# Performance work log

Hardware: AMD Instinct MI355X
Metric: run time of the kernel (lower is better)

The kernel has to match this reference:

```python
import jax, jax.numpy as jnp
import numpy as np

K = 20          # neighbors per point (knn includes the point itself, as in PyG knn)
EPS = 1e-5      # BatchNorm eps (eval mode, running stats)


def _lrelu(x):
    return jax.nn.leaky_relu(x, 0.2)


def _bn(x, g, beta, mu, var):
    # eval-mode BatchNorm1d over last (feature) axis
    return (x - mu) * (g * jax.lax.rsqrt(var + EPS)) + beta


def _edge_conv(x, W, g, beta, mu, var):
    # x: [B, N, F]. Dynamic kNN graph per batch element, edge feature [x_i, x_j - x_i],
    # Linear(no bias) -> BN -> LeakyReLU(0.2), max-aggregate over neighbors.
    sq = jnp.sum(x * x, axis=-1)                                   # [B, N]
    d2 = sq[:, :, None] + sq[:, None, :] - 2.0 * jnp.einsum('bnf,bmf->bnm', x, x)
    _, idx = jax.lax.top_k(-d2, K)                                 # [B, N, K] (self is nearest)
    xj = jax.vmap(lambda xb, ib: xb[ib])(x, idx)                   # [B, N, K, F]
    xi = jnp.broadcast_to(x[:, :, None, :], xj.shape)
    e = jnp.concatenate([xi, xj - xi], axis=-1) @ W                # [B, N, K, out]
    return jnp.max(_lrelu(_bn(e, g, beta, mu, var)), axis=2)       # [B, N, out]


def setup_inputs() -> dict:
    key = jax.random.key(0)
    ks = iter(jax.random.split(key, 64))
    B, N = 8, 2048
    d = {"pos": jax.random.normal(next(ks), (B, N, 3), jnp.float32)}

    def bn_params(name, dim):
        d["g" + name] = 0.5 + jax.random.uniform(next(ks), (dim,), jnp.float32)
        d["beta" + name] = 0.1 * jax.random.normal(next(ks), (dim,), jnp.float32)
        d["mu" + name] = 0.1 * jax.random.normal(next(ks), (dim,), jnp.float32)
        d["var" + name] = 0.5 + jax.random.uniform(next(ks), (dim,), jnp.float32)

    def lin(name, din, dout):
        d["W" + name] = jax.random.normal(next(ks), (din, dout), jnp.float32) / np.sqrt(din).astype(np.float32)

    lin("1", 2 * 3, 64);    bn_params("1", 64)
    lin("2", 2 * 64, 64);   bn_params("2", 64)
    lin("3", 2 * 64, 128);  bn_params("3", 128)
    lin("4", 2 * 128, 256); bn_params("4", 256)
    lin("m", 512, 1024);    bn_params("m", 1024)
    lin("a", 2048, 512);    bn_params("a", 512)
    lin("b", 512, 256);     bn_params("b", 256)
    d["bias_b"] = 0.01 * jax.random.normal(next(ks), (256,), jnp.float32)
    lin("c", 256, 40)
    d["bias_c"] = 0.01 * jax.random.normal(next(ks), (40,), jnp.float32)
    return d


def reference(pos, W1, g1, beta1, mu1, var1, W2, g2, beta2, mu2, var2,
              W3, g3, beta3, mu3, var3, W4, g4, beta4, mu4, var4,
              Wm, gm, betam, mum, varm, Wa, ga, betaa, mua, vara,
              Wb, gb, betab, mub, varb, bias_b, Wc, bias_c):
    x1 = _edge_conv(pos, W1, g1, beta1, mu1, var1)   # [B, N, 64]
    x2 = _edge_conv(x1, W2, g2, beta2, mu2, var2)    # [B, N, 64]
    x3 = _edge_conv(x2, W3, g3, beta3, mu3, var3)    # [B, N, 128]
    x4 = _edge_conv(x3, W4, g4, beta4, mu4, var4)    # [B, N, 256]
    h = jnp.concatenate([x1, x2, x3, x4], axis=-1)   # [B, N, 512]
    h = _lrelu(_bn(h @ Wm, gm, betam, mum, varm))    # [B, N, 1024]
    pooled = jnp.concatenate([jnp.max(h, axis=1), jnp.mean(h, axis=1)], axis=-1)  # [B, 2048]
    h = _lrelu(_bn(pooled @ Wa, ga, betaa, mua, vara))            # [B, 512]
    h = _lrelu(_bn(h @ Wb + bias_b, gb, betab, mub, varb))        # [B, 256]
    return h @ Wc + bias_c                                        # [B, 40]
```

## Files before the change

### kernel.cpp

```cpp
#include <hip/hip_runtime.h>
#include <cstdint>
#include <cstddef>

#define NPTS 2048
#define BATCH 8
#define KNN 20
#define BIGF 3.402823466e38f

typedef short bf16x8 __attribute__((ext_vector_type(8)));
typedef float f32x4 __attribute__((ext_vector_type(4)));

__device__ __forceinline__ unsigned short f2bf(float v) {
    uint32_t u = __float_as_uint(v);
    uint32_t r = (u + 0x7FFFu + ((u >> 16) & 1u)) >> 16;
    return (unsigned short)r;
}
__device__ __forceinline__ float bf2f(unsigned short h) {
    return __uint_as_float(((uint32_t)h) << 16);
}
__device__ __forceinline__ uint32_t flipkey(float d) {
    uint32_t u = __float_as_uint(d);
    return (u & 0x80000000u) ? ~u : (u | 0x80000000u);
}
__device__ __forceinline__ uint64_t shfl_xor_u64(uint64_t v, int m) {
    int lo = __shfl_xor((int)(uint32_t)v, m, 64);
    int hi = __shfl_xor((int)(uint32_t)(v >> 32), m, 64);
    return ((uint64_t)(uint32_t)hi << 32) | (uint32_t)lo;
}

__global__ __launch_bounds__(256) void sq_kernel(const float* __restrict__ x, int lda, int F,
                                                 float* __restrict__ sq)
{
    int p = blockIdx.x * 256 + threadIdx.x;
    const float* xp = x + (size_t)p * lda;
    float s = 0.f;
    for (int f = 0; f < F; ++f) { float v = xp[f]; s = fmaf(v, v, s); }
    sq[p] = s;
}

__global__ __launch_bounds__(256) void distk_kernel(const float* __restrict__ x, int lda,
                                                    const float* __restrict__ sq,
                                                    uint32_t* __restrict__ d2k, int F, int b0)
{
    __shared__ __align__(16) float As[8][132];
    __shared__ __align__(16) float Bs[8][132];
    const int b  = b0 + blockIdx.z;
    const int i0 = blockIdx.x * 128;
    const int j0 = blockIdx.y * 128;
    const float* xb  = x + (size_t)b * NPTS * lda;
    const float* sqb = sq + (size_t)b * NPTS;
    const int t  = threadIdx.x;
    const int tx = t & 15, ty = t >> 4;
    const int lrow = t >> 1, lkq = (t & 1) * 4;

    float acc[8][8];
#pragma unroll
    for (int r = 0; r < 8; ++r)
#pragma unroll
        for (int c = 0; c < 8; ++c) acc[r][c] = 0.f;

    for (int k0 = 0; k0 < F; k0 += 8) {
        const float* sa = xb + (size_t)(i0 + lrow) * lda + k0 + lkq;
        const float* sb = xb + (size_t)(j0 + lrow) * lda + k0 + lkq;
        if (k0 + 8 <= F) {
            float4 a4 = *reinterpret_cast<const float4*>(sa);
            float4 b4 = *reinterpret_cast<const float4*>(sb);
            As[lkq + 0][lrow] = a4.x; As[lkq + 1][lrow] = a4.y;
            As[lkq + 2][lrow] = a4.z; As[lkq + 3][lrow] = a4.w;
            Bs[lkq + 0][lrow] = b4.x; Bs[lkq + 1][lrow] = b4.y;
            Bs[lkq + 2][lrow] = b4.z; Bs[lkq + 3][lrow] = b4.w;
        } else {
#pragma unroll
            for (int q = 0; q < 4; ++q) {
                int kk = k0 + lkq + q;
                As[lkq + q][lrow] = (kk < F) ? sa[q] : 0.f;
                Bs[lkq + q][lrow] = (kk < F) ? sb[q] : 0.f;
            }
        }
        __syncthreads();
#pragma unroll
        for (int k = 0; k < 8; ++k) {
            float4 a0 = *reinterpret_cast<const float4*>(&As[k][ty * 4]);
            float4 a1 = *reinterpret_cast<const float4*>(&As[k][64 + ty * 4]);
            float4 c0 = *reinterpret_cast<const float4*>(&Bs[k][tx * 4]);
            float4 c1 = *reinterpret_cast<const float4*>(&Bs[k][64 + tx * 4]);
            float av[8] = {a0.x, a0.y, a0.z, a0.w, a1.x, a1.y, a1.z, a1.w};
            float bv[8] = {c0.x, c0.y, c0.z, c0.w, c1.x, c1.y, c1.z, c1.w};
#pragma unroll
            for (int r = 0; r < 8; ++r)
#pragma unroll
                for (int c = 0; c < 8; ++c) acc[r][c] = fmaf(av[r], bv[c], acc[r][c]);
        }
        __syncthreads();
    }

    uint32_t* db = d2k + (size_t)blockIdx.z * NPTS * NPTS;
#pragma unroll
    for (int r = 0; r < 8; ++r) {
        int i = i0 + ((r < 4) ? (ty * 4 + r) : (64 + ty * 4 + r - 4));
        float si = sqb[i];
#pragma unroll
        for (int cq = 0; cq < 2; ++cq) {
            int j = j0 + (cq ? 64 : 0) + tx * 4;
            uint4 o;
            o.x = flipkey(si + sqb[j + 0] - 2.f * acc[r][cq * 4 + 0]);
            o.y = flipkey(si + sqb[j + 1] - 2.f * acc[r][cq * 4 + 1]);
            o.z = flipkey(si + sqb[j + 2] - 2.f * acc[r][cq * 4 + 2]);
            o.w = flipkey(si + sqb[j + 3] - 2.f * acc[r][cq * 4 + 3]);
            *reinterpret_cast<uint4*>(&db[(size_t)i * NPTS + j]) = o;
        }
    }
}

__global__ __launch_bounds__(256) void select_kernel(const uint32_t* __restrict__ d2k,
                                                     int* __restrict__ idx, int b0)
{
    const int t    = threadIdx.x;
    const int lane = t & 63;
    const int wid  = t >> 6;
    const int row_id = blockIdx.x * 4 + wid;
    const int bz = row_id >> 11;
    const int i  = row_id & 2047;
    const uint32_t* row = d2k + ((size_t)bz * NPTS + i) * NPTS;

    uint32_t key[32];
#pragma unroll
    for (int s = 0; s < 8; ++s) {
        uint4 kv = *reinterpret_cast<const uint4*>(&row[s * 256 + lane * 4]);
        key[s * 4 + 0] = kv.x; key[s * 4 + 1] = kv.y;
        key[s * 4 + 2] = kv.z; key[s * 4 + 3] = kv.w;
    }

    const uint64_t MAXV = ~0ull;
    uint64_t t1 = MAXV, t2 = MAXV, t3 = MAXV, t4 = MAXV;

#pragma unroll
    for (int s = 0; s < 8; ++s)
#pragma unroll
        for (int q = 0; q < 4; ++q) {
            uint64_t c = ((uint64_t)key[s * 4 + q] << 32) | (uint32_t)(s * 256 + lane * 4 + q);
            if (c < t4) {
                if (c < t2) {
                    t4 = t3; t3 = t2;
                    if (c < t1) { t2 = t1; t1 = c; } else t2 = c;
                } else {
                    if (c < t3) { t4 = t3; t3 = c; } else t4 = c;
                }
            }
        }

    uint64_t keep = 0;
    for (int it = 0; it < KNN; ++it) {
        uint64_t w = t1;
#pragma unroll
        for (int o = 1; o < 64; o <<= 1) {
            uint64_t ov = shfl_xor_u64(w, o);
            w = (ov < w) ? ov : w;
        }
        keep = (lane == it) ? w : keep;
        if (t1 == w) {
            t1 = t2; t2 = t3; t3 = t4; t4 = MAXV;
            if (t1 == MAXV) {
#pragma unroll
                for (int s = 0; s < 8; ++s)
#pragma unroll
                    for (int q = 0; q < 4; ++q) {
                        uint64_t c = ((uint64_t)key[s * 4 + q] << 32) |
                                     (uint32_t)(s * 256 + lane * 4 + q);
                        if (c > w && c < t4) {
                            if (c < t2) {
                                t4 = t3; t3 = t2;
                                if (c < t1) { t2 = t1; t1 = c; } else t2 = c;
                            } else {
                                if (c < t3) { t4 = t3; t3 = c; } else t4 = c;
                            }
                        }
                    }
            }
        }
    }

    int* out = idx + ((size_t)(b0 + bz) * NPTS + i) * KNN;
    if (lane < KNN) out[lane] = (int)(uint32_t)keep;
}

__global__ __launch_bounds__(256) void gemm64_kernel(const float* __restrict__ A, int lda, int F,
                                                     const float* __restrict__ Wfull, int Fout,
                                                     float* __restrict__ apart,
                                                     float* __restrict__ bpart)
{
    __shared__ float As[16][65];
    __shared__ float Bs[16][65];
    const int i0 = blockIdx.x * 64, j0 = blockIdx.y * 64;
    const int half = blockIdx.z;
    const float* Bw = Wfull + (size_t)(half ? F : 0) * Fout;
    float* C = half ? bpart : apart;
    const int t = threadIdx.x, tx = t & 15, ty = t >> 4;
    float acc[4][4];
#pragma unroll
    for (int r = 0; r < 4; ++r)
#pragma unroll
        for (int c = 0; c < 4; ++c) acc[r][c] = 0.f;
    const int arow = t >> 2, akq = (t & 3) * 4;
    const int bk = t >> 4, bj = (t & 15) * 4;
    for (int k0 = 0; k0 < F; k0 += 16) {
#pragma unroll
        for (int q = 0; q < 4; ++q) {
            int kk = k0 + akq + q;
            As[akq + q][arow] = (kk < F) ? A[(size_t)(i0 + arow) * lda + kk] : 0.f;
        }
        {
            int kk = k0 + bk;
#pragma unroll
            for (int q = 0; q < 4; ++q)
                Bs[bk][bj + q] = (kk < F) ? Bw[(size_t)kk * Fout + j0 + bj + q] : 0.f;
        }
        __syncthreads();
#pragma unroll
        for (int k = 0; k < 16; ++k) {
            float a[4], bb[4];
#pragma unroll
            for (int r = 0; r < 4; ++r) a[r] = As[k][ty * 4 + r];
#pragma unroll
            for (int c = 0; c < 4; ++c) bb[c] = Bs[k][tx * 4 + c];
#pragma unroll
            for (int r = 0; r < 4; ++r)
#pragma unroll
                for (int c = 0; c < 4; ++c) acc[r][c] = fmaf(a[r], bb[c], acc[r][c]);
        }
        __syncthreads();
    }
#pragma unroll
    for (int r = 0; r < 4; ++r)
#pragma unroll
        for (int c = 0; c < 4; ++c)
            C[(size_t)(i0 + ty * 4 + r) * Fout + j0 + tx * 4 + c] = acc[r][c];
}

template <int FOUT>
__global__ __launch_bounds__(256) void aggregate_kernel(const float* __restrict__ apart,
                                                        const float* __restrict__ bpart,
                                                        const int* __restrict__ idx,
                                                        const float* __restrict__ g,
                                                        const float* __restrict__ be,
                                                        const float* __restrict__ mu,
                                                        const float* __restrict__ var,
                                                        float* __restrict__ out)
{
    constexpr int G   = FOUT / 4;
    constexpr int PPB = 256 / G;
    const int t  = threadIdx.x;
    const int pi = t / G;
    const int fi = t % G;
    const int p  = blockIdx.x * PPB + pi;
    const int b  = p >> 11;
    const int* nb = idx + (size_t)p * KNN;
    const float4* bp4 = reinterpret_cast<const float4*>(bpart);
    const float4* bb  = bp4 + ((size_t)b << 11) * G;

    float4 m = {-BIGF, -BIGF, -BIGF, -BIGF};
#pragma unroll 4
    for (int k = 0; k < KNN; ++k) {
        int j = nb[k];
        float4 v = bb[(size_t)j * G + fi];
        m.x = fmaxf(m.x, v.x); m.y = fmaxf(m.y, v.y);
        m.z = fmaxf(m.z, v.z); m.w = fmaxf(m.w, v.w);
    }
    float4 av = reinterpret_cast<const float4*>(apart)[(size_t)p * G + fi];
    float4 bv = bp4[(size_t)p * G + fi];
    float4 gg = reinterpret_cast<const float4*>(g)[fi];
    float4 bee = reinterpret_cast<const float4*>(be)[fi];
    float4 muu = reinterpret_cast<const float4*>(mu)[fi];
    float4 vaa = reinterpret_cast<const float4*>(var)[fi];

    float4 r;
    {
        float s, sh, vv, y;
        s = gg.x * rsqrtf(vaa.x + 1e-5f); sh = bee.x - muu.x * s;
        vv = av.x - bv.x + m.x; y = vv * s + sh; r.x = (y >= 0.f) ? y : 0.2f * y;
        s = gg.y * rsqrtf(vaa.y + 1e-5f); sh = bee.y - muu.y * s;
        vv = av.y - bv.y + m.y; y = vv * s + sh; r.y = (y >= 0.f) ? y : 0.2f * y;
        s = gg.z * rsqrtf(vaa.z + 1e-5f); sh = bee.z - muu.z * s;
        vv = av.z - bv.z + m.z; y = vv * s + sh; r.z = (y >= 0.f) ? y : 0.2f * y;
        s = gg.w * rsqrtf(vaa.w + 1e-5f); sh = bee.w - muu.w * s;
        vv = av.w - bv.w + m.w; y = vv * s + sh; r.w = (y >= 0.f) ? y : 0.2f * y;
    }
    *reinterpret_cast<float4*>(out + (size_t)p * 512 + fi * 4) = r;
}

__global__ __launch_bounds__(256) void cvt_kernel(const float* __restrict__ in,
                                                  unsigned short* __restrict__ hi,
                                                  unsigned short* __restrict__ lo)
{
    int i = blockIdx.x * 256 + threadIdx.x;
    const float4* p = reinterpret_cast<const float4*>(in) + (size_t)i * 2;
    float4 a = p[0], b = p[1];
    float v[8] = {a.x, a.y, a.z, a.w, b.x, b.y, b.z, b.w};
    uint32_t h[8], l[8];
#pragma unroll
    for (int q = 0; q < 8; ++q) {
        unsigned short hb = f2bf(v[q]);
        h[q] = hb;
        l[q] = f2bf(v[q] - bf2f(hb));
    }
    uint4 uh, ul;
    uh.x = h[0] | (h[1] << 16); uh.y = h[2] | (h[3] << 16);
    uh.z = h[4] | (h[5] << 16); uh.w = h[6] | (h[7] << 16);
    ul.x = l[0] | (l[1] << 16); ul.y = l[2] | (l[3] << 16);
    ul.z = l[4] | (l[5] << 16); ul.w = l[6] | (l[7] << 16);
    reinterpret_cast<uint4*>(hi)[i] = uh;
    reinterpret_cast<uint4*>(lo)[i] = ul;
}

__global__ __launch_bounds__(256) void cvtT_kernel(const float* __restrict__ Wm,
                                                   unsigned short* __restrict__ hiT,
                                                   unsigned short* __restrict__ loT)
{
    __shared__ float tile[32][33];
    const int n0 = blockIdx.x * 32;
    const int k0 = blockIdx.y * 32;
    const int t = threadIdx.x;
    const int c = t & 31, r = t >> 5;
#pragma unroll
    for (int rr = 0; rr < 4; ++rr)
        tile[r + rr * 8][c] = Wm[(size_t)(k0 + r + rr * 8) * 1024 + n0 + c];
    __syncthreads();
#pragma unroll
    for (int rr = 0; rr < 4; ++rr) {
        int nn = r + rr * 8, kk = c;
        float v = tile[kk][nn];
        unsigned short hb = f2bf(v);
        hiT[(size_t)(n0 + nn) * 512 + k0 + kk] = hb;
        loT[(size_t)(n0 + nn) * 512 + k0 + kk] = f2bf(v - bf2f(hb));
    }
}

__global__ __launch_bounds__(256) void wm_mfma_pool(const unsigned short* __restrict__ AH,
                                                    const unsigned short* __restrict__ AL,
                                                    const unsigned short* __restrict__ BH,
                                                    const unsigned short* __restrict__ BL,
                                                    const float* __restrict__ g,
                                                    const float* __restrict__ be,
                                                    const float* __restrict__ mu,
                                                    const float* __restrict__ var,
                                                    float* __restrict__ partmax,
                                                    float* __restrict__ partsum)
{
    __shared__ unsigned short AsH[128][40], AsL[128][40], BsH[128][40], BsL[128][40];
    __shared__ float redm[4][64], reds[4][64];
    const int t = threadIdx.x;
    const int i0 = blockIdx.x * 128, j0 = blockIdx.y * 128;
    const int lane = t & 63, wid = t >> 6, wy = wid >> 1, wx = wid & 1;
    const int lc = lane & 15, kg = lane >> 4;

    f32x4 acc[4][4];
#pragma unroll
    for (int mi = 0; mi < 4; ++mi)
#pragma unroll
        for (int ni = 0; ni < 4; ++ni) acc[mi][ni] = (f32x4){0.f, 0.f, 0.f, 0.f};

    for (int k0 = 0; k0 < 512; k0 += 32) {
        __syncthreads();
#pragma unroll
        for (int q = 0; q < 2; ++q) {
            int c = t + q * 256;
            int row = c >> 2, ko = (c & 3) * 8;
            *reinterpret_cast<uint4*>(&AsH[row][ko]) =
                *reinterpret_cast<const uint4*>(&AH[(size_t)(i0 + row) * 512 + k0 + ko]);
            *reinterpret_cast<uint4*>(&AsL[row][ko]) =
                *reinterpret_cast<const uint4*>(&AL[(size_t)(i0 + row) * 512 + k0 + ko]);
            *reinterpret_cast<uint4*>(&BsH[row][ko]) =
                *reinterpret_cast<const uint4*>(&BH[(size_t)(j0 + row) * 512 + k0 + ko]);
            *reinterpret_cast<uint4*>(&BsL[row][ko]) =
                *reinterpret_cast<const uint4*>(&BL[(size_t)(j0 + row) * 512 + k0 + ko]);
        }
        __syncthreads();

        bf16x8 aH[4], aL[4], bH[4], bL[4];
#pragma unroll
        for (int mi = 0; mi < 4; ++mi) {
            int ar = wy * 64 + mi * 16 + lc;
            aH[mi] = *reinterpret_cast<const bf16x8*>(&AsH[ar][kg * 8]);
            aL[mi] = *reinterpret_cast<const bf16x8*>(&AsL[ar][kg * 8]);
        }
#pragma unroll
        for (int ni = 0; ni < 4; ++ni) {
            int br = wx * 64 + ni * 16 + lc;
            bH[ni] = *reinterpret_cast<const bf16x8*>(&BsH[br][kg * 8]);
            bL[ni] = *reinterpret_cast<const bf16x8*>(&BsL[br][kg * 8]);
        }
#pragma unroll
        for (int mi = 0; mi < 4; ++mi)
#pragma unroll
            for (int ni = 0; ni < 4; ++ni) {
                acc[mi][ni] = __builtin_amdgcn_mfma_f32_16x16x32_bf16(aH[mi], bH[ni], acc[mi][ni], 0, 0, 0);
                acc[mi][ni] = __builtin_amdgcn_mfma_f32_16x16x32_bf16(aH[mi], bL[ni], acc[mi][ni], 0, 0, 0);
                acc[mi][ni] = __builtin_amdgcn_mfma_f32_16x16x32_bf16(aL[mi], bH[ni], acc[mi][ni], 0, 0, 0);
            }
    }

    float pmax[4], psum[4];
#pragma unroll
    for (int ni = 0; ni < 4; ++ni) {
        int j = j0 + wx * 64 + ni * 16 + lc;
        float s = g[j] * rsqrtf(var[j] + 1e-5f);
        float sh = be[j] - mu[j] * s;
        float pm = -BIGF, ps = 0.f;
#pragma unroll
        for (int mi = 0; mi < 4; ++mi)
#pragma unroll
            for (int r = 0; r < 4; ++r) {
                float y = fmaf(acc[mi][ni][r], s, sh);
                y = (y >= 0.f) ? y : 0.2f * y;
                pm = fmaxf(pm, y);
                ps += y;
            }
        pmax[ni] = pm; psum[ni] = ps;
    }
#pragma unroll
    for (int ni = 0; ni < 4; ++ni) {
        pmax[ni] = fmaxf(pmax[ni], __shfl_xor(pmax[ni], 16, 64));
        pmax[ni] = fmaxf(pmax[ni], __shfl_xor(pmax[ni], 32, 64));
        psum[ni] += __shfl_xor(psum[ni], 16, 64);
        psum[ni] += __shfl_xor(psum[ni], 32, 64);
    }
    if (lane < 16) {
#pragma unroll
        for (int ni = 0; ni < 4; ++ni) {
            redm[wid][ni * 16 + lc] = pmax[ni];
            reds[wid][ni * 16 + lc] = psum[ni];
        }
    }
    __syncthreads();
    if (t < 128) {
        int wxq = t >> 6, cl = t & 63;
        float m = fmaxf(redm[wxq][cl], redm[2 + wxq][cl]);
        float sv = reds[wxq][cl] + reds[2 + wxq][cl];
        int b = i0 >> 11, rb = (i0 & 2047) >> 7;
        partmax[((size_t)b * 16 + rb) * 1024 + j0 + t] = m;
        partsum[((size_t)b * 16 + rb) * 1024 + j0 + t] = sv;
    }
}

__global__ __launch_bounds__(256) void pool2_kernel(const float* __restrict__ partmax,
                                                    const float* __restrict__ partsum,
                                                    float* __restrict__ pooled)
{
    const int c = blockIdx.x * 256 + threadIdx.x;
    const int b = blockIdx.y;
    float m = -BIGF, s = 0.f;
    for (int rb = 0; rb < 16; ++rb) {
        m = fmaxf(m, partmax[((size_t)b * 16 + rb) * 1024 + c]);
        s += partsum[((size_t)b * 16 + rb) * 1024 + c];
    }
    pooled[(size_t)b * 2048 + c] = m;
    pooled[(size_t)b * 2048 + 1024 + c] = s * (1.f / 2048.f);
}

__global__ __launch_bounds__(512) void fc1_partial(const float* __restrict__ pooled,
                                                   const float* __restrict__ Wa,
                                                   float* __restrict__ part)
{
    const int kk = blockIdx.x, b = blockIdx.y, c = threadIdx.x;
    __shared__ float sp[128];
    if (c < 128) sp[c] = pooled[(size_t)b * 2048 + kk * 128 + c];
    __syncthreads();
    const float* w = Wa + (size_t)kk * 128 * 512 + c;
    float acc = 0.f;
#pragma unroll 8
    for (int j = 0; j < 128; ++j) acc = fmaf(sp[j], w[(size_t)j * 512], acc);
    part[((size_t)b * 16 + kk) * 512 + c] = acc;
}

__global__ __launch_bounds__(512) void fc1_reduce(const float* __restrict__ part,
                                                  const float* __restrict__ g, const float* __restrict__ be,
                                                  const float* __restrict__ mu, const float* __restrict__ var,
                                                  float* __restrict__ t1)
{
    const int b = blockIdx.x, c = threadIdx.x;
    float acc = 0.f;
#pragma unroll
    for (int kk = 0; kk < 16; ++kk) acc += part[((size_t)b * 16 + kk) * 512 + c];
    float s = g[c] * rsqrtf(var[c] + 1e-5f);
    float y = acc * s + (be[c] - mu[c] * s);
    t1[(size_t)b * 512 + c] = (y >= 0.f) ? y : 0.2f * y;
}

__global__ __launch_bounds__(256) void fc2_partial(const float* __restrict__ t1,
                                                   const float* __restrict__ Wb,
                                                   float* __restrict__ part)
{
    const int kk = blockIdx.x, b = blockIdx.y, c = threadIdx.x;
    __shared__ float sp[128];
    if (c < 128) sp[c] = t1[(size_t)b * 512 + kk * 128 + c];
    __syncthreads();
    const float* w = Wb + (size_t)kk * 128 * 256 + c;
    float acc = 0.f;
#pragma unroll 8
    for (int j = 0; j < 128; ++j) acc = fmaf(sp[j], w[(size_t)j * 256], acc);
    part[((size_t)b * 4 + kk) * 256 + c] = acc;
}

__global__ __launch_bounds__(256) void fc2_reduce(const float* __restrict__ part,
                                                  const float* __restrict__ bias_b,
                                                  const float* __restrict__ g, const float* __restrict__ be,
                                                  const float* __restrict__ mu, const float* __restrict__ var,
                                                  float* __restrict__ t2)
{
    const int b = blockIdx.x, c = threadIdx.x;
    float acc = bias_b[c];
#pragma unroll
    for (int kk = 0; kk < 4; ++kk) acc += part[((size_t)b * 4 + kk) * 256 + c];
    float s = g[c] * rsqrtf(var[c] + 1e-5f);
    float y = acc * s + (be[c] - mu[c] * s);
    t2[(size_t)b * 256 + c] = (y >= 0.f) ? y : 0.2f * y;
}

__global__ __launch_bounds__(64) void fc3_kernel(const float* __restrict__ t2,
                                                 const float* __restrict__ Wc,
                                                 const float* __restrict__ bias_c,
                                                 float* __restrict__ out)
{
    const int b = blockIdx.x, c = threadIdx.x;
    __shared__ float sp[256];
    for (int k = c; k < 256; k += 64) sp[k] = t2[(size_t)b * 256 + k];
    __syncthreads();
    if (c < 40) {
        float acc = 0.f;
#pragma unroll 8
        for (int k = 0; k < 256; ++k) acc = fmaf(sp[k], Wc[(size_t)k * 40 + c], acc);
        out[(size_t)b * 40 + c] = acc + bias_c[c];
    }
}

extern "C" void kernel_launch(void* const* d_in, const int* in_sizes, int n_in,
                              void* d_out, int out_size, void* d_ws, size_t ws_size,
                              hipStream_t stream)
{
    const float* pos = (const float*)d_in[0];
    const float* W1 = (const float*)d_in[1];
    const float* g1 = (const float*)d_in[2];  const float* be1 = (const float*)d_in[3];
    const float* mu1 = (const float*)d_in[4]; const float* va1 = (const float*)d_in[5];
    const float* W2 = (const float*)d_in[6];
    const float* g2 = (const float*)d_in[7];  const float* be2 = (const float*)d_in[8];
    const float* mu2 = (const float*)d_in[9]; const float* va2 = (const float*)d_in[10];
    const float* W3 = (const float*)d_in[11];
    const float* g3 = (const float*)d_in[12]; const float* be3 = (const float*)d_in[13];
    const float* mu3 = (const float*)d_in[14];const float* va3 = (const float*)d_in[15];
    const float* W4 = (const float*)d_in[16];
    const float* g4 = (const float*)d_in[17]; const float* be4 = (const float*)d_in[18];
    const float* mu4 = (const float*)d_in[19];const float* va4 = (const float*)d_in[20];
    const float* Wm = (const float*)d_in[21];
    const float* gm = (const float*)d_in[22]; const float* bem = (const float*)d_in[23];
    const float* mum = (const float*)d_in[24];const float* vam = (const float*)d_in[25];
    const float* Wa = (const float*)d_in[26];
    const float* ga = (const float*)d_in[27]; const float* bea = (const float*)d_in[28];
    const float* mua = (const float*)d_in[29];const float* vaa = (const float*)d_in[30];
    const float* Wb = (const float*)d_in[31];
    const float* gb = (const float*)d_in[32]; const float* beb = (const float*)d_in[33];
    const float* mub = (const float*)d_in[34];const float* vab = (const float*)d_in[35];
    const float* bias_b = (const float*)d_in[36];
    const float* Wc = (const float*)d_in[37];
    const float* bias_c = (const float*)d_in[38];

    char* ws = (char*)d_ws;
    size_t off = 0;
    auto alloc = [&](size_t bytes) -> void* {
        void* p = ws + off;
        off += (bytes + 255) & ~(size_t)255;
        return p;
    };
    float* xcat    = (float*)alloc((size_t)16384 * 512 * 4);
    float* sq      = (float*)alloc((size_t)16384 * 4);
    int*   idx     = (int*)  alloc((size_t)16384 * KNN * 4);
    float* apart   = (float*)alloc((size_t)16384 * 256 * 4);
    float* bpart   = (float*)alloc((size_t)16384 * 256 * 4);
    float* partmax = (float*)alloc((size_t)8 * 16 * 1024 * 4);
    float* partsum = (float*)alloc((size_t)8 * 16 * 1024 * 4);
    float* pooled  = (float*)alloc((size_t)8 * 2048 * 4);
    float* t1      = (float*)alloc((size_t)8 * 512 * 4);
    float* t2      = (float*)alloc((size_t)8 * 256 * 4);
    float* part1   = (float*)alloc((size_t)8 * 16 * 512 * 4);
    float* part2   = (float*)alloc((size_t)8 * 4 * 256 * 4);
    unsigned short* ah   = (unsigned short*)alloc((size_t)16384 * 512 * 2);
    unsigned short* al   = (unsigned short*)alloc((size_t)16384 * 512 * 2);
    unsigned short* wmtH = (unsigned short*)alloc((size_t)1024 * 512 * 2);
    unsigned short* wmtL = (unsigned short*)alloc((size_t)1024 * 512 * 2);
    const size_t fixed = off;
    const size_t per_b = (size_t)NPTS * NPTS * 4;

    int CB; uint32_t* d2k;
    if      (ws_size >= fixed + 4 * per_b) { CB = 4; d2k = (uint32_t*)(ws + fixed); }
    else if (ws_size >= fixed + 2 * per_b) { CB = 2; d2k = (uint32_t*)(ws + fixed); }
    else { CB = 2; d2k = (uint32_t*)apart; }

    struct LayerDesc {
        const float* xin; int lda; int F; int Fout;
        float* xout; const float* W;
        const float* g; const float* be; const float* mu; const float* va;
    };
    LayerDesc Ls[4] = {
        { pos,        3,   3,   64,  xcat + 0,   W1, g1, be1, mu1, va1 },
        { xcat + 0,   512, 64,  64,  xcat + 64,  W2, g2, be2, mu2, va2 },
        { xcat + 64,  512, 64,  128, xcat + 128, W3, g3, be3, mu3, va3 },
        { xcat + 128, 512, 128, 256, xcat + 256, W4, g4, be4, mu4, va4 },
    };

    for (int L = 0; L < 4; ++L) {
        const LayerDesc& ld = Ls[L];
        sq_kernel<<<64, 256, 0, stream>>>(ld.xin, ld.lda, ld.F, sq);
        for (int b0 = 0; b0 < BATCH; b0 += CB) {
            int cb = (BATCH - b0 < CB) ? (BATCH - b0) : CB;
            distk_kernel<<<dim3(16, 16, cb), 256, 0, stream>>>(ld.xin, ld.lda, sq, d2k, ld.F, b0);
            select_kernel<<<512 * cb, 256, 0, stream>>>(d2k, idx, b0);
        }
        gemm64_kernel<<<dim3(256, ld.Fout / 64, 2), 256, 0, stream>>>(
            ld.xin, ld.lda, ld.F, ld.W, ld.Fout, apart, bpart);
        if (ld.Fout == 64)
            aggregate_kernel<64><<<1024, 256, 0, stream>>>(apart, bpart, idx,
                ld.g, ld.be, ld.mu, ld.va, ld.xout);
        else if (ld.Fout == 128)
            aggregate_kernel<128><<<2048, 256, 0, stream>>>(apart, bpart, idx,
                ld.g, ld.be, ld.mu, ld.va, ld.xout);
        else
            aggregate_kernel<256><<<4096, 256, 0, stream>>>(apart, bpart, idx,
                ld.g, ld.be, ld.mu, ld.va, ld.xout);
    }

    cvt_kernel<<<4096, 256, 0, stream>>>(xcat, ah, al);
    cvtT_kernel<<<dim3(32, 16), 256, 0, stream>>>(Wm, wmtH, wmtL);
    wm_mfma_pool<<<dim3(128, 8), 256, 0, stream>>>(ah, al, wmtH, wmtL,
                                                   gm, bem, mum, vam, partmax, partsum);
    pool2_kernel<<<dim3(4, 8), 256, 0, stream>>>(partmax, partsum, pooled);
    fc1_partial<<<dim3(16, 8), 512, 0, stream>>>(pooled, Wa, part1);
    fc1_reduce<<<8, 512, 0, stream>>>(part1, ga, bea, mua, vaa, t1);
    fc2_partial<<<dim3(4, 8), 256, 0, stream>>>(t1, Wb, part2);
    fc2_reduce<<<8, 256, 0, stream>>>(part2, bias_b, gb, beb, mub, vab, t2);
    fc3_kernel<<<8, 64, 0, stream>>>(t2, Wc, bias_c, (float*)d_out);
}
```

Baseline: 1.002 ms.

## Store distance keys as 16-bit and refine boundary ties with exact recompute

The distance kernel now writes only the top 16 bits of each order-preserving distance key, halving the size of the N×N distance buffer. The select kernel packs a 16-bit key and a 16-bit index into 32-bit candidates for a cheaper 32-bit top-k shuffle. Where the truncated key ties at the kth boundary, it recomputes exact fp32 distances for just those candidates to resolve the order. Halving the buffer lets more batches run per chunk, at the cost of extra branchy code and occasional slow paths.

```diff
diff --git a/kernel.cpp b/kernel.cpp
--- a/kernel.cpp
+++ b/kernel.cpp
@@ -21,6 +21,9 @@
 __device__ __forceinline__ uint32_t flipkey(float d) {
     uint32_t u = __float_as_uint(d);
     return (u & 0x80000000u) ? ~u : (u | 0x80000000u);
+}
+__device__ __forceinline__ uint32_t d2key(float acc, float si, float sj) {
+    return flipkey(fmaf(-2.f, acc, si + sj));
 }
 __device__ __forceinline__ uint64_t shfl_xor_u64(uint64_t v, int m) {
     int lo = __shfl_xor((int)(uint32_t)v, m, 64);
@@ -40,7 +43,8 @@
 
 __global__ __launch_bounds__(256) void distk_kernel(const float* __restrict__ x, int lda,
                                                     const float* __restrict__ sq,
-                                                    uint32_t* __restrict__ d2k, int F, int b0)
+                                                    unsigned short* __restrict__ d2u16,
+                                                    int F, int b0)
 {
     __shared__ __align__(16) float As[8][132];
     __shared__ __align__(16) float Bs[8][132];
@@ -94,7 +98,7 @@
         __syncthreads();
     }
 
-    uint32_t* db = d2k + (size_t)blockIdx.z * NPTS * NPTS;
+    unsigned short* db = d2u16 + (size_t)blockIdx.z * NPTS * NPTS;
 #pragma unroll
     for (int r = 0; r < 8; ++r) {
         int i = i0 + ((r < 4) ? (ty * 4 + r) : (64 + ty * 4 + r - 4));
@@ -102,17 +106,20 @@
 #pragma unroll
         for (int cq = 0; cq < 2; ++cq) {
             int j = j0 + (cq ? 64 : 0) + tx * 4;
-            uint4 o;
-            o.x = flipkey(si + sqb[j + 0] - 2.f * acc[r][cq * 4 + 0]);
-            o.y = flipkey(si + sqb[j + 1] - 2.f * acc[r][cq * 4 + 1]);
-            o.z = flipkey(si + sqb[j + 2] - 2.f * acc[r][cq * 4 + 2]);
-            o.w = flipkey(si + sqb[j + 3] - 2.f * acc[r][cq * 4 + 3]);
-            *reinterpret_cast<uint4*>(&db[(size_t)i * NPTS + j]) = o;
-        }
-    }
-}
-
-__global__ __launch_bounds__(256) void select_kernel(const uint32_t* __restrict__ d2k,
+            ushort4 o;
+            o.x = (unsigned short)(d2key(acc[r][cq * 4 + 0], si, sqb[j + 0]) >> 16);
+            o.y = (unsigned short)(d2key(acc[r][cq * 4 + 1], si, sqb[j + 1]) >> 16);
+            o.z = (unsigned short)(d2key(acc[r][cq * 4 + 2], si, sqb[j + 2]) >> 16);
+            o.w = (unsigned short)(d2key(acc[r][cq * 4 + 3], si, sqb[j + 3]) >> 16);
+            *reinterpret_cast<ushort4*>(&db[(size_t)i * NPTS + j]) = o;
+        }
+    }
+}
+
+template <int F>
+__global__ __launch_bounds__(256) void select_kernel(const unsigned short* __restrict__ d2u16,
+                                                     const float* __restrict__ x, int lda,
+                                                     const float* __restrict__ sq,
                                                      int* __restrict__ idx, int b0)
 {
     const int t    = threadIdx.x;
@@ -121,67 +128,141 @@
     const int row_id = blockIdx.x * 4 + wid;
     const int bz = row_id >> 11;
     const int i  = row_id & 2047;
-    const uint32_t* row = d2k + ((size_t)bz * NPTS + i) * NPTS;
-
-    uint32_t key[32];
-#pragma unroll
-    for (int s = 0; s < 8; ++s) {
-        uint4 kv = *reinterpret_cast<const uint4*>(&row[s * 256 + lane * 4]);
-        key[s * 4 + 0] = kv.x; key[s * 4 + 1] = kv.y;
-        key[s * 4 + 2] = kv.z; key[s * 4 + 3] = kv.w;
-    }
-
-    const uint64_t MAXV = ~0ull;
-    uint64_t t1 = MAXV, t2 = MAXV, t3 = MAXV, t4 = MAXV;
-
-#pragma unroll
-    for (int s = 0; s < 8; ++s)
-#pragma unroll
-        for (int q = 0; q < 4; ++q) {
-            uint64_t c = ((uint64_t)key[s * 4 + q] << 32) | (uint32_t)(s * 256 + lane * 4 + q);
-            if (c < t4) {
-                if (c < t2) {
-                    t4 = t3; t3 = t2;
-                    if (c < t1) { t2 = t1; t1 = c; } else t2 = c;
-                } else {
-                    if (c < t3) { t4 = t3; t3 = c; } else t4 = c;
-                }
+    const unsigned short* row = d2u16 + ((size_t)bz * NPTS + i) * NPTS;
+
+    uint32_t cand[32];
+#pragma unroll
+    for (int s = 0; s < 4; ++s) {
+        uint4 kv = *reinterpret_cast<const uint4*>(&row[s * 512 + lane * 8]);
+        uint32_t cb = (uint32_t)(s * 512 + lane * 8);
+        cand[s * 8 + 0] = ((kv.x & 0xFFFFu) << 16) | (cb + 0);
+        cand[s * 8 + 1] = (kv.x & 0xFFFF0000u)      | (cb + 1);
+        cand[s * 8 + 2] = ((kv.y & 0xFFFFu) << 16) | (cb + 2);
+        cand[s * 8 + 3] = (kv.y & 0xFFFF0000u)      | (cb + 3);
+        cand[s * 8 + 4] = ((kv.z & 0xFFFFu) << 16) | (cb + 4);
+        cand[s * 8 + 5] = (kv.z & 0xFFFF0000u)      | (cb + 5);
+        cand[s * 8 + 6] = ((kv.w & 0xFFFFu) << 16) | (cb + 6);
+        cand[s * 8 + 7] = (kv.w & 0xFFFF0000u)      | (cb + 7);
+    }
+
+    const uint32_t MAXV = 0xFFFFFFFFu;
+    uint32_t t1 = MAXV, t2 = MAXV, t3 = MAXV, t4 = MAXV;
+#pragma unroll
+    for (int s = 0; s < 32; ++s) {
+        uint32_t c = cand[s];
+        if (c < t4) {
+            if (c < t2) {
+                t4 = t3; t3 = t2;
+                if (c < t1) { t2 = t1; t1 = c; } else t2 = c;
+            } else {
+                if (c < t3) { t4 = t3; t3 = c; } else t4 = c;
             }
         }
-
-    uint64_t keep = 0;
+    }
+
+    uint32_t keep = 0, last = 0;
     for (int it = 0; it < KNN; ++it) {
-        uint64_t w = t1;
-#pragma unroll
-        for (int o = 1; o < 64; o <<= 1) {
-            uint64_t ov = shfl_xor_u64(w, o);
-            w = (ov < w) ? ov : w;
-        }
+        uint32_t w = t1;
+#pragma unroll
+        for (int o = 1; o < 64; o <<= 1)
+            w = min(w, (uint32_t)__shfl_xor((int)w, o, 64));
         keep = (lane == it) ? w : keep;
+        last = w;
         if (t1 == w) {
             t1 = t2; t2 = t3; t3 = t4; t4 = MAXV;
             if (t1 == MAXV) {
 #pragma unroll
-                for (int s = 0; s < 8; ++s)
-#pragma unroll
-                    for (int q = 0; q < 4; ++q) {
-                        uint64_t c = ((uint64_t)key[s * 4 + q] << 32) |
-                                     (uint32_t)(s * 256 + lane * 4 + q);
-                        if (c > w && c < t4) {
-                            if (c < t2) {
-                                t4 = t3; t3 = t2;
-                                if (c < t1) { t2 = t1; t1 = c; } else t2 = c;
-                            } else {
-                                if (c < t3) { t4 = t3; t3 = c; } else t4 = c;
-                            }
+                for (int s = 0; s < 32; ++s) {
+                    uint32_t c = cand[s];
+                    if (c > w && c < t4) {
+                        if (c < t2) {
+                            t4 = t3; t3 = t2;
+                            if (c < t1) { t2 = t1; t1 = c; } else t2 = c;
+                        } else {
+                            if (c < t3) { t4 = t3; t3 = c; } else t4 = c;
                         }
                     }
+                }
             }
         }
     }
 
     int* out = idx + ((size_t)(b0 + bz) * NPTS + i) * KNN;
-    if (lane < KNN) out[lane] = (int)(uint32_t)keep;
+    const uint32_t thr16 = last >> 16;
+
+    int cnt = 0;
+#pragma unroll
+    for (int s = 0; s < 32; ++s) cnt += ((cand[s] >> 16) == thr16) ? 1 : 0;
+#pragma unroll
+    for (int o = 1; o < 64; o <<= 1) cnt += __shfl_xor(cnt, o, 64);
+
+    unsigned long long bm = __ballot(lane < KNN && (keep >> 16) < thr16);
+    const int sel_lt = (int)__popcll(bm);
+    const int m = KNN - sel_lt;
+    const bool fast = (cnt == m);
+
+    if (lane < KNN && (fast || (keep >> 16) < thr16))
+        out[lane] = (int)(keep & 0xFFFFu);
+    if (fast) return;
+
+    const float* xb  = x + (size_t)(b0 + bz) * NPTS * lda;
+    const float* sqb = sq + (size_t)(b0 + bz) * NPTS;
+    const float si = sqb[i];
+    const float* xi = xb + (size_t)i * lda;
+
+    uint64_t tc[4]; int ntc = 0; bool ovf = false;
+#pragma unroll
+    for (int s = 0; s < 32; ++s) {
+        if ((cand[s] >> 16) == thr16) {
+            if (ntc < 4) {
+                int j = (int)(cand[s] & 0xFFFFu);
+                const float* xj = xb + (size_t)j * lda;
+                float dot = 0.f;
+#pragma unroll
+                for (int k = 0; k < F; ++k) dot = fmaf(xi[k], xj[k], dot);
+                uint32_t fk = d2key(dot, si, sqb[j]);
+                tc[ntc++] = ((uint64_t)fk << 32) | (uint32_t)j;
+            } else ovf = true;
+        }
+    }
+    if (__ballot(ovf)) {
+        uint64_t last_ex = 0;
+        for (int q = 0; q < m; ++q) {
+            uint64_t lm = ~0ull;
+            for (int s = 0; s < 32; ++s) {
+                if ((cand[s] >> 16) == thr16) {
+                    int j = (int)(cand[s] & 0xFFFFu);
+                    const float* xj = xb + (size_t)j * lda;
+                    float dot = 0.f;
+                    for (int k = 0; k < F; ++k) dot = fmaf(xi[k], xj[k], dot);
+                    uint64_t e = ((uint64_t)d2key(dot, si, sqb[j]) << 32) | (uint32_t)j;
+                    if (e > last_ex && e < lm) lm = e;
+                }
+            }
+#pragma unroll
+            for (int o = 1; o < 64; o <<= 1) {
+                uint64_t ov = shfl_xor_u64(lm, o);
+                lm = (ov < lm) ? ov : lm;
+            }
+            if (lane == 0) out[sel_lt + q] = (int)(lm & 0xFFFFu);
+            last_ex = lm;
+        }
+        return;
+    }
+    uint64_t last_ex = 0;
+    for (int q = 0; q < m; ++q) {
+        uint64_t lm = ~0ull;
+#pragma unroll
+        for (int u = 0; u < 4; ++u)
+            if (u < ntc && tc[u] > last_ex && tc[u] < lm) lm = tc[u];
+#pragma unroll
+        for (int o = 1; o < 64; o <<= 1) {
+            uint64_t ov = shfl_xor_u64(lm, o);
+            lm = (ov < lm) ? ov : lm;
+        }
+        if (lane == 0) out[sel_lt + q] = (int)(lm & 0xFFFFu);
+        last_ex = lm;
+    }
 }
 
 __global__ __launch_bounds__(256) void gemm64_kernel(const float* __restrict__ A, int lda, int F,
@@ -189,7 +270,7 @@
                                                      float* __restrict__ apart,
                                                      float* __restrict__ bpart)
 {
-    __shared__ float As[16][65];
+    __shared__ float As[16][68];
     __shared__ float Bs[16][65];
     const int i0 = blockIdx.x * 64, j0 = blockIdx.y * 64;
     const int half = blockIdx.z;
@@ -587,12 +668,12 @@
     unsigned short* wmtH = (unsigned short*)alloc((size_t)1024 * 512 * 2);
     unsigned short* wmtL = (unsigned short*)alloc((size_t)1024 * 512 * 2);
     const size_t fixed = off;
-    const size_t per_b = (size_t)NPTS * NPTS * 4;
-
-    int CB; uint32_t* d2k;
-    if      (ws_size >= fixed + 4 * per_b) { CB = 4; d2k = (uint32_t*)(ws + fixed); }
-    else if (ws_size >= fixed + 2 * per_b) { CB = 2; d2k = (uint32_t*)(ws + fixed); }
-    else { CB = 2; d2k = (uint32_t*)apart; }
+    const size_t per_b16 = (size_t)NPTS * NPTS * 2;
+
+    int CB; unsigned short* d2u16;
+    if      (ws_size >= fixed + 8 * per_b16) { CB = 8; d2u16 = (unsigned short*)(ws + fixed); }
+    else if (ws_size >= fixed + 4 * per_b16) { CB = 4; d2u16 = (unsigned short*)(ws + fixed); }
+    else { CB = 4; d2u16 = (unsigned short*)apart; }
 
     struct LayerDesc {
         const float* xin; int lda; int F; int Fout;
@@ -611,8 +692,13 @@
         sq_kernel<<<64, 256, 0, stream>>>(ld.xin, ld.lda, ld.F, sq);
         for (int b0 = 0; b0 < BATCH; b0 += CB) {
             int cb = (BATCH - b0 < CB) ? (BATCH - b0) : CB;
-            distk_kernel<<<dim3(16, 16, cb), 256, 0, stream>>>(ld.xin, ld.lda, sq, d2k, ld.F, b0);
-            select_kernel<<<512 * cb, 256, 0, stream>>>(d2k, idx, b0);
+            distk_kernel<<<dim3(16, 16, cb), 256, 0, stream>>>(ld.xin, ld.lda, sq, d2u16, ld.F, b0);
+            if (ld.F == 3)
+                select_kernel<3><<<512 * cb, 256, 0, stream>>>(d2u16, ld.xin, ld.lda, sq, idx, b0);
+            else if (ld.F == 64)
+                select_kernel<64><<<512 * cb, 256, 0, stream>>>(d2u16, ld.xin, ld.lda, sq, idx, b0);
+            else
+                select_kernel<128><<<512 * cb, 256, 0, stream>>>(d2u16, ld.xin, ld.lda, sq, idx, b0);
         }
         gemm64_kernel<<<dim3(256, ld.Fout / 64, 2), 256, 0, stream>>>(
             ld.xin, ld.lda, ld.F, ld.W, ld.Fout, apart, bpart);
```

After: 856.7 us. -14.5%, faster.
